# Optimization experiments

Hardware: AMD Instinct MI355X
Metric: run time of the kernel (lower is better)

The kernel has to match this reference:

```python
import jax, jax.numpy as jnp
import numpy as np

B, C, N, T = 32, 32, 512, 168
EMB = 40
K_NEI = 20
ALPHA = 3.0          # saturation rate in graph learning
GCN_DEPTH = 2
PROP_ALPHA = 0.05    # retaining ratio in mix-hop propagation
KERNELS = (2, 3, 6, 7)
DIL = 2
T_OUT = T - (max(KERNELS) - 1) * DIL   # 156
C_BR = C // len(KERNELS)               # 8 channels per inception branch
EPS = 1e-5


def _conv2d(x, w, b, dil):
    # x: (B,Cin,N,T), w: (Cout,Cin,1,k), temporal dilation dil
    y = jax.lax.conv_general_dilated(
        x, w, window_strides=(1, 1), padding='VALID',
        rhs_dilation=(1, dil), dimension_numbers=('NCHW', 'OIHW', 'NCHW'))
    return y + b[None, :, None, None]


def _inception(x, ws, bs):
    outs = [_conv2d(x, w, b, DIL) for w, b in zip(ws, bs)]
    tmin = outs[-1].shape[-1]   # largest kernel -> shortest output
    return jnp.concatenate([o[..., -tmin:] for o in outs], axis=1)


def setup_inputs() -> dict:
    key = jax.random.key(0)
    ks = jax.random.split(key, 32)
    d = {}
    d['x'] = jax.random.normal(ks[0], (B, C, N, T), jnp.float32)
    d['idx'] = jnp.arange(N)  # permutation of nodes (identity)
    # graph learning params
    d['emb1'] = jax.random.normal(ks[1], (N, EMB), jnp.float32)
    d['emb2'] = jax.random.normal(ks[2], (N, EMB), jnp.float32)
    d['W1'] = jax.random.normal(ks[3], (EMB, EMB), jnp.float32) * 0.15
    d['b1'] = jnp.zeros((EMB,), jnp.float32)
    d['W2'] = jax.random.normal(ks[4], (EMB, EMB), jnp.float32) * 0.15
    d['b2'] = jnp.zeros((EMB,), jnp.float32)
    # dilated inception filter/gate conv params
    i = 5
    for pre in ('f', 'g'):
        for k in KERNELS:
            d[f'{pre}w{k}'] = jax.random.normal(ks[i], (C_BR, C, 1, k), jnp.float32) * 0.05
            d[f'{pre}b{k}'] = jnp.zeros((C_BR,), jnp.float32)
            i += 1
    # mix-hop 1x1 mlp: (gcn_depth+1)*C -> C
    d['mlp_w'] = jax.random.normal(ks[i], (C, (GCN_DEPTH + 1) * C, 1, 1), jnp.float32) * 0.05
    d['mlp_b'] = jnp.zeros((C,), jnp.float32)
    # node-indexed layer norm affine params, shape (C, N, T_OUT)
    d['ln_w'] = jnp.ones((C, N, T_OUT), jnp.float32)
    d['ln_b'] = jnp.zeros((C, N, T_OUT), jnp.float32)
    return d


def reference(x, idx, emb1, emb2, W1, b1, W2, b2,
              fw2, fb2, fw3, fb3, fw6, fb6, fw7, fb7,
              gw2, gb2, gw3, gb3, gw6, gb6, gw7, gb7,
              mlp_w, mlp_b, ln_w, ln_b):
    # ---- graph learning: topk-masked adjacency (N,N) ----
    n1 = jnp.tanh(ALPHA * (emb1[idx] @ W1.T + b1))
    n2 = jnp.tanh(ALPHA * (emb2[idx] @ W2.T + b2))
    a = n1 @ n2.T - n2 @ n1.T
    A = jax.nn.relu(jnp.tanh(ALPHA * a))
    _, top_idx = jax.lax.top_k(A, K_NEI)                 # deterministic topk (torch adds rand*0.01 tiebreak)
    mask = jnp.zeros_like(A).at[jnp.arange(A.shape[0])[:, None], top_idx].set(1.0)
    A = A * mask

    # ---- dilated inception gated temporal conv ----
    filt = jnp.tanh(_inception(x, (fw2, fw3, fw6, fw7), (fb2, fb3, fb6, fb7)))
    gate = jax.nn.sigmoid(_inception(x, (gw2, gw3, gw6, gw7), (gb2, gb3, gb6, gb7)))
    z = filt * gate                                       # (B, C, N, T_OUT)

    # ---- mix-hop graph convolution ----
    Ah = A + jnp.eye(A.shape[0], dtype=A.dtype)
    Ah = Ah / Ah.sum(1, keepdims=True)                    # row-degree normalization
    h = z
    hops = [z]
    for _ in range(GCN_DEPTH):
        h = PROP_ALPHA * z + (1.0 - PROP_ALPHA) * jnp.einsum('bcwt,vw->bcvt', h, Ah)
        hops.append(h)
    h0 = jnp.concatenate(hops, axis=1)                    # (B, 3C, N, T_OUT)
    out = _conv2d(h0, mlp_w, mlp_b, 1)                    # 1x1 mlp -> (B, C, N, T_OUT)

    # ---- residual + node-indexed layer norm over dims (C,N,T) ----
    out = out + x[..., -T_OUT:]
    mean = out.mean(axis=(1, 2, 3), keepdims=True)
    var = out.var(axis=(1, 2, 3), keepdims=True)
    out = (out - mean) * jax.lax.rsqrt(var + EPS)
    out = out * ln_w[:, idx, :][None] + ln_b[:, idx, :][None]
    return out
```

## Files before the change

kernel.cpp:

```cpp
#include <hip/hip_runtime.h>

#define NB 32
#define NC 32
#define NNODE 512
#define NT 168
#define NTO 156
#define NQ 39
#define NEMB 40
#define KNEI 20
#define NADJ 21
#define ZT_PITCH 42
#define XROWS 176
#define NPB 4
#define CT (NC * NTO)
#define NPAIR (CT / 8)

static_assert(NTO == 4 * NQ, "t quads");

typedef __attribute__((ext_vector_type(8))) short bf16x8;
typedef __attribute__((ext_vector_type(16))) float f32x16;
typedef __attribute__((ext_vector_type(4))) float f32x4;
typedef __attribute__((ext_vector_type(8))) unsigned short u16x8;

__device__ __forceinline__ float fast_tanh(float x) {
  float e = __expf(2.0f * x);
  return 1.0f - 2.0f / (e + 1.0f);
}
__device__ __forceinline__ float fast_sigmoid(float x) {
  return 1.0f / (1.0f + __expf(-x));
}
__device__ __forceinline__ unsigned short f2b(float v) {
  unsigned int u = __float_as_uint(v);
  unsigned int r = (u + 0x7FFFu + ((u >> 16) & 1u)) >> 16;
  return (unsigned short)r;
}
__device__ __forceinline__ float b2f(unsigned short u) {
  return __uint_as_float((unsigned int)u << 16);
}
template <typename T>
__device__ __forceinline__ void pin(T& v) {
  f32x4 t = __builtin_bit_cast(f32x4, v);
  asm volatile("" : "+v"(t));
  v = __builtin_bit_cast(T, t);
}

__global__ __launch_bounds__(128) void g1_kernel(
    const float* __restrict__ emb1, const float* __restrict__ emb2,
    const float* __restrict__ W1, const float* __restrict__ b1,
    const float* __restrict__ W2, const float* __restrict__ b2,
    const int* __restrict__ idx, float* __restrict__ n1, float* __restrict__ n2) {
  const int v = blockIdx.x;
  const int tid = threadIdx.x;
  const int iv = idx[v];
  if (tid < NEMB) {
    float s = b1[tid];
    const float* er = emb1 + iv * NEMB;
    const float* wr = W1 + tid * NEMB;
    for (int f = 0; f < NEMB; ++f) s = fmaf(er[f], wr[f], s);
    n1[v * NEMB + tid] = tanhf(3.0f * s);
  } else if (tid >= 64 && tid < 64 + NEMB) {
    const int e = tid - 64;
    float s = b2[e];
    const float* er = emb2 + iv * NEMB;
    const float* wr = W2 + e * NEMB;
    for (int f = 0; f < NEMB; ++f) s = fmaf(er[f], wr[f], s);
    n2[v * NEMB + e] = tanhf(3.0f * s);
  }
}

__global__ __launch_bounds__(256) void g2_kernel(
    const float* __restrict__ n1, const float* __restrict__ n2,
    int* __restrict__ cols, float* __restrict__ wts) {
  const int v = blockIdx.x;
  const int tid = threadIdx.x;
  volatile __shared__ float Arow[NNODE];
  __shared__ float n1v[NEMB], n2v[NEMB];
  if (tid < NEMB) n1v[tid] = n1[v * NEMB + tid];
  if (tid >= 64 && tid < 64 + NEMB) n2v[tid - 64] = n2[v * NEMB + tid - 64];
  __syncthreads();
  for (int w = tid; w < NNODE; w += 256) {
    float d1 = 0.f, d2 = 0.f;
    const float* r1 = n1 + w * NEMB;
    const float* r2 = n2 + w * NEMB;
    for (int e = 0; e < NEMB; ++e) {
      d1 = fmaf(n1v[e], r2[e], d1);
      d2 = fmaf(n2v[e], r1[e], d2);
    }
    float a = tanhf(3.0f * (d1 - d2));
    Arow[w] = a > 0.f ? a : 0.f;
  }
  __syncthreads();
  if (tid >= 64) return;
  float sum = 1.0f;
  float selv[KNEI];
  int seli[KNEI];
  #pragma unroll
  for (int s = 0; s < KNEI; ++s) {
    float bv = -1.f; int bi = NNODE;
    #pragma unroll
    for (int w8 = 0; w8 < NNODE / 64; ++w8) {
      const int w = tid + 64 * w8;
      const float val = Arow[w];
      if (val > bv || (val == bv && w < bi)) { bv = val; bi = w; }
    }
    #pragma unroll
    for (int off = 32; off >= 1; off >>= 1) {
      const float ov = __shfl_down(bv, off);
      const int oi = __shfl_down(bi, off);
      if (ov > bv || (ov == bv && oi < bi)) { bv = ov; bi = oi; }
    }
    bv = __shfl(bv, 0);
    bi = __shfl(bi, 0);
    selv[s] = bv;
    seli[s] = bi;
    Arow[bi] = -2.f;
    sum += bv;
  }
  if (tid == 0) {
    const float inv = 1.0f / sum;
    #pragma unroll
    for (int s = 0; s < KNEI; ++s) {
      cols[v * NADJ + s] = seli[s];
      wts[v * NADJ + s] = selv[s] * inv;
    }
    cols[v * NADJ + KNEI] = v;
    wts[v * NADJ + KNEI] = inv;
  }
}

struct ZParams {
  const float* fw[4]; const float* fb[4];
  const float* gw[4]; const float* gb[4];
};

#define PA_CNT (2 * 2 * 7 * 64 * 8)
#define PB_CNT (2 * 64 * 16)
#define PNA_CNT (3 * 2 * 64 * 8)
__global__ __launch_bounds__(256) void pack_kernel(ZParams p, const float* __restrict__ mw,
                                                   unsigned short* __restrict__ pA,
                                                   float* __restrict__ pB,
                                                   unsigned short* __restrict__ pNA) {
  const int idx = blockIdx.x * 256 + threadIdx.x;
  if (idx < PA_CNT) {
    const int e = idx & 7;
    const int l = (idx >> 3) & 63;
    int rest = idx >> 9;
    const int j = rest % 7;
    rest /= 7;
    const int s = rest & 1;
    const int m = rest >> 1;
    const int row = l & 31;
    const int k = ((l >> 5) << 3) + e;
    const int ci = s * 16 + k;
    const int isF = (row < 16);
    const int co = m * 16 + (isF ? row : row - 16);
    const int br = co >> 3;
    const int kk = (br == 0) ? 2 : (br == 1) ? 3 : (br == 2) ? 6 : 7;
    const int jw = j - (7 - kk);
    const float* arr = isF ? p.fw[br] : p.gw[br];
    float val = (jw >= 0) ? arr[((co & 7) * NC + ci) * kk + jw] : 0.f;
    pA[idx] = f2b(val);
  } else if (idx < PA_CNT + PB_CNT) {
    const int ib = idx - PA_CNT;
    const int r = ib & 15;
    const int l = (ib >> 4) & 63;
    const int m = ib >> 10;
    const int rr = r & 7;
    const int row = (rr & 3) + 8 * (rr >> 2) + 4 * (l >> 5);
    const int co = m * 16 + row;
    const int br = co >> 3;
    const float* arr = (r < 8) ? p.fb[br] : p.gb[br];
    pB[ib] = arr[co & 7];
  } else if (idx < PA_CNT + PB_CNT + PNA_CNT) {
    const int in_ = idx - (PA_CNT + PB_CNT);
    const int e = in_ & 7;
    const int l = (in_ >> 3) & 63;
    const int s = (in_ >> 9) & 1;
    const int which = in_ >> 10;
    const int co = l & 31;
    const int c = s * 16 + ((l >> 5) << 3) + e;
    const float w0 = mw[co * 96 + c];
    const float w1 = mw[co * 96 + 32 + c];
    const float w2 = mw[co * 96 + 64 + c];
    float val;
    if (which == 0)      val = w0 + 0.05f * (w1 + w2);
    else if (which == 1) val = 0.95f * w1 + 0.0475f * w2;
    else                 val = 0.9025f * w2;
    pNA[in_] = f2b(val);
  }
}

__global__ __launch_bounds__(256) void xprep_kernel(
    const float* __restrict__ x, unsigned short* __restrict__ xbf) {
  const int n = blockIdx.x;
  const int b = blockIdx.y;
  const int tid = threadIdx.x;
  const int cp = tid & 15;
  const int t0 = tid >> 4;
  const float* xc0 = x + ((size_t)(b * NC + 2 * cp) * NNODE + n) * NT;
  const float* xc1 = xc0 + (size_t)NNODE * NT;
  unsigned int* dst = (unsigned int*)(xbf + (size_t)(b * NNODE + n) * (XROWS * NC));
  #pragma unroll
  for (int k = 0; k < 11; ++k) {
    const int t = t0 + 16 * k;
    unsigned int v = 0;
    if (t < NT) {
      v = (unsigned int)f2b(xc0[t]) | ((unsigned int)f2b(xc1[t]) << 16);
    }
    dst[t * 16 + cp] = v;
  }
}

__attribute__((amdgpu_waves_per_eu(2)))
__global__ __launch_bounds__(256) void conv_kernel(
    const unsigned short* __restrict__ xbf, const unsigned short* __restrict__ pA,
    const float* __restrict__ pBias, unsigned short* __restrict__ z) {
  __shared__ unsigned short zt[NTO * ZT_PITCH];
  const int n0 = blockIdx.x * NPB;
  const int b = blockIdx.y;
  const int tid = threadIdx.x;
  const int w = tid >> 6, l = tid & 63;
  const int jc = l & 31, h = l >> 5;
  const int m = w & 1;

  bf16x8 aF[2][7];
  #pragma unroll
  for (int s = 0; s < 2; ++s)
    #pragma unroll
    for (int j = 0; j < 7; ++j) {
      aF[s][j] = *reinterpret_cast<const bf16x8*>(
          pA + ((((m * 2 + s) * 7 + j) << 6) + l) * 8);
      pin(aF[s][j]);
    }
  f32x4 bias4[4];
  {
    const f32x4* pb4 = reinterpret_cast<const f32x4*>(pBias + (m * 64 + l) * 16);
    #pragma unroll
    for (int q = 0; q < 4; ++q) { bias4[q] = pb4[q]; pin(bias4[q]); }
  }

  for (int nn = 0; nn < NPB; ++nn) {
    const int n = n0 + nn;
    const unsigned short* xbn = xbf + (size_t)(b * NNODE + n) * (XROWS * NC);
    for (int tile = (w >> 1); tile < 5; tile += 2) {
      const int t0 = tile * 32;
      f32x16 acc;
      #pragma unroll
      for (int r = 0; r < 16; ++r) acc[r] = bias4[r >> 2][r & 3];
      const unsigned short* bp = xbn + (t0 + jc) * NC + h * 8;
      #pragma unroll
      for (int j = 0; j < 7; ++j) {
        bf16x8 b0 = *reinterpret_cast<const bf16x8*>(bp + 2 * j * NC);
        bf16x8 b1 = *reinterpret_cast<const bf16x8*>(bp + 2 * j * NC + 16);
        acc = __builtin_amdgcn_mfma_f32_32x32x16_bf16(aF[0][j], b0, acc, 0, 0, 0);
        acc = __builtin_amdgcn_mfma_f32_32x32x16_bf16(aF[1][j], b1, acc, 0, 0, 0);
      }
      const int t = t0 + jc;
      if (t < NTO) {
        #pragma unroll
        for (int r = 0; r < 8; ++r) {
          const float f = fast_tanh(acc[r]);
          const float g = fast_sigmoid(acc[r + 8]);
          const int row = (r & 3) + 8 * (r >> 2) + 4 * h;
          const int co = m * 16 + row;
          zt[t * ZT_PITCH + co] = f2b(f * g);
        }
      }
    }
    __syncthreads();
    unsigned short* zv = z + (size_t)(b * NNODE + n) * CT;
    for (int i = tid; i < CT / 4; i += 256) {
      const int row = i >> 3, q = i & 7;
      ushort4 v4 = *reinterpret_cast<const ushort4*>(zt + row * ZT_PITCH + 4 * q);
      *reinterpret_cast<ushort4*>(zv + 4 * i) = v4;
    }
    __syncthreads();
  }
}

__global__ __launch_bounds__(256) void hop_kernel(
    const unsigned short* __restrict__ src, const int* __restrict__ cols,
    const float* __restrict__ wts, unsigned short* __restrict__ dst) {
  const int bid = blockIdx.x;
  const int v = bid & (NNODE - 1);
  const int b = bid >> 9;
  const int tid = threadIdx.x;
  float acc[3][8];
  #pragma unroll
  for (int k = 0; k < 3; ++k)
    #pragma unroll
    for (int j = 0; j < 8; ++j) acc[k][j] = 0.f;
  for (int s = 0; s < NADJ; ++s) {
    const int col = cols[v * NADJ + s];
    const float w = wts[v * NADJ + s];
    const unsigned short* p = src + ((size_t)(b << 9) + col) * CT;
    #pragma unroll
    for (int k = 0; k < 2; ++k) {
      u16x8 u = *reinterpret_cast<const u16x8*>(p + 8 * (tid + 256 * k));
      #pragma unroll
      for (int j = 0; j < 8; ++j) acc[k][j] = fmaf(w, b2f(u[j]), acc[k][j]);
    }
    if (tid < NPAIR - 512) {
      u16x8 u = *reinterpret_cast<const u16x8*>(p + 8 * (tid + 512));
      #pragma unroll
      for (int j = 0; j < 8; ++j) acc[2][j] = fmaf(w, b2f(u[j]), acc[2][j]);
    }
  }
  unsigned short* dp = dst + ((size_t)(b << 9) + v) * CT;
  #pragma unroll
  for (int k = 0; k < 2; ++k) {
    u16x8 o;
    #pragma unroll
    for (int j = 0; j < 8; ++j) o[j] = f2b(acc[k][j]);
    *reinterpret_cast<u16x8*>(dp + 8 * (tid + 256 * k)) = o;
  }
  if (tid < NPAIR - 512) {
    u16x8 o;
    #pragma unroll
    for (int j = 0; j < 8; ++j) o[j] = f2b(acc[2][j]);
    *reinterpret_cast<u16x8*>(dp + 8 * (tid + 512)) = o;
  }
}

__global__ __launch_bounds__(256) void fin_kernel(
    const unsigned short* __restrict__ z, const unsigned short* __restrict__ g1,
    const unsigned short* __restrict__ g2, const float* __restrict__ x,
    const unsigned short* __restrict__ pNA, const float* __restrict__ mb,
    unsigned short* __restrict__ P, float* __restrict__ stats) {
  const int b = blockIdx.y;
  const int tid = threadIdx.x;
  const int w = tid >> 6, l = tid & 63;
  const int jc = l & 31, h = l >> 5;
  const int v = blockIdx.x * 4 + w;

  bf16x8 nA[3][2];
  #pragma unroll
  for (int which = 0; which < 3; ++which)
    #pragma unroll
    for (int s = 0; s < 2; ++s) {
      nA[which][s] = *reinterpret_cast<const bf16x8*>(
          pNA + (((which * 2 + s) << 6) + l) * 8);
      pin(nA[which][s]);
    }
  float mbr[16];
  #pragma unroll
  for (int r = 0; r < 16; ++r) {
    const int co = (r & 3) + 8 * (r >> 2) + 4 * h;
    mbr[r] = mb[co];
  }

  const size_t base = (size_t)(b << 9) + v;
  const unsigned short* zs_ = z + base * CT;
  const unsigned short* g1s = g1 + base * CT;
  const unsigned short* g2s = g2 + base * CT;
  unsigned short* Ps = P + base * CT;
  float st1 = 0.f, st2 = 0.f;

  #pragma unroll
  for (int tile = 0; tile < 5; ++tile) {
    const int t = tile * 32 + jc;
    const int off = t * NC + h * 8;
    f32x16 acc;
    #pragma unroll
    for (int r = 0; r < 16; ++r) acc[r] = 0.f;
    {
      bf16x8 b0 = *reinterpret_cast<const bf16x8*>(zs_ + off);
      bf16x8 b1 = *reinterpret_cast<const bf16x8*>(zs_ + off + 16);
      acc = __builtin_amdgcn_mfma_f32_32x32x16_bf16(nA[0][0], b0, acc, 0, 0, 0);
      acc = __builtin_amdgcn_mfma_f32_32x32x16_bf16(nA[0][1], b1, acc, 0, 0, 0);
    }
    {
      bf16x8 b0 = *reinterpret_cast<const bf16x8*>(g1s + off);
      bf16x8 b1 = *reinterpret_cast<const bf16x8*>(g1s + off + 16);
      acc = __builtin_amdgcn_mfma_f32_32x32x16_bf16(nA[1][0], b0, acc, 0, 0, 0);
      acc = __builtin_amdgcn_mfma_f32_32x32x16_bf16(nA[1][1], b1, acc, 0, 0, 0);
    }
    {
      bf16x8 b0 = *reinterpret_cast<const bf16x8*>(g2s + off);
      bf16x8 b1 = *reinterpret_cast<const bf16x8*>(g2s + off + 16);
      acc = __builtin_amdgcn_mfma_f32_32x32x16_bf16(nA[2][0], b0, acc, 0, 0, 0);
      acc = __builtin_amdgcn_mfma_f32_32x32x16_bf16(nA[2][1], b1, acc, 0, 0, 0);
    }
    if (t < NTO) {
      #pragma unroll
      for (int r = 0; r < 16; ++r) {
        const int co = (r & 3) + 8 * (r >> 2) + 4 * h;
        const float xr = x[((size_t)(b * NC + co) * NNODE + v) * NT + 12 + t];
        const float val = acc[r] + mbr[r] + xr;
        Ps[co * NTO + t] = f2b(val);
        st1 += val;
        st2 += val * val;
      }
    }
  }
  #pragma unroll
  for (int off = 32; off >= 1; off >>= 1) {
    st1 += __shfl_down(st1, off);
    st2 += __shfl_down(st2, off);
  }
  __shared__ float r1[4], r2[4];
  if ((tid & 63) == 0) { r1[w] = st1; r2[w] = st2; }
  __syncthreads();
  if (tid == 0) {
    atomicAdd(&stats[b * 2], r1[0] + r1[1] + r1[2] + r1[3]);
    atomicAdd(&stats[b * 2 + 1], r2[0] + r2[1] + r2[2] + r2[3]);
  }
}

__global__ __launch_bounds__(256) void ln_kernel(
    const unsigned short* __restrict__ P, float* __restrict__ out,
    const float* __restrict__ lnw, const float* __restrict__ lnb,
    const int* __restrict__ idx, const float* __restrict__ stats) {
  const int i = blockIdx.x * 256 + threadIdx.x;
  const int q = i % NQ;
  const int r = i / NQ;
  const int co = r % NC;
  const int r2 = r / NC;
  const int v = r2 % NNODE;
  const int b = r2 / NNODE;
  const float invM = 1.0f / (float)(NC * NNODE * NTO);
  const float mean = stats[b * 2] * invM;
  const float var = stats[b * 2 + 1] * invM - mean * mean;
  const float rs = rsqrtf(var + 1e-5f);
  ushort4 u = *reinterpret_cast<const ushort4*>(P + 4 * i);
  const int iv = idx[v];
  const int lb = (co * NNODE + iv) * NTO + 4 * q;
  const float4 w = *reinterpret_cast<const float4*>(lnw + lb);
  const float4 bb = *reinterpret_cast<const float4*>(lnb + lb);
  float4 o;
  o.x = (b2f(u.x) - mean) * rs * w.x + bb.x;
  o.y = (b2f(u.y) - mean) * rs * w.y + bb.y;
  o.z = (b2f(u.z) - mean) * rs * w.z + bb.z;
  o.w = (b2f(u.w) - mean) * rs * w.w + bb.w;
  const int ob = ((b * NC + co) * NNODE + v) * NTO + 4 * q;
  *reinterpret_cast<float4*>(out + ob) = o;
}

extern "C" void kernel_launch(void* const* d_in, const int* in_sizes, int n_in,
                              void* d_out, int out_size, void* d_ws, size_t ws_size,
                              hipStream_t stream) {
  const float* x    = (const float*)d_in[0];
  const int*   idx  = (const int*)d_in[1];
  const float* emb1 = (const float*)d_in[2];
  const float* emb2 = (const float*)d_in[3];
  const float* W1   = (const float*)d_in[4];
  const float* b1   = (const float*)d_in[5];
  const float* W2   = (const float*)d_in[6];
  const float* b2   = (const float*)d_in[7];
  const float* mlp_w = (const float*)d_in[24];
  const float* mlp_b = (const float*)d_in[25];
  const float* ln_w = (const float*)d_in[26];
  const float* ln_b = (const float*)d_in[27];

  char* ws = (char*)d_ws;
  float* n1    = (float*)(ws);
  float* n2    = (float*)(ws + (128 << 10));
  int*   cols  = (int*)  (ws + (256 << 10));
  float* wts   = (float*)(ws + (320 << 10));
  float* stats = (float*)(ws + (384 << 10));
  unsigned short* pA = (unsigned short*)(ws + (400 << 10));
  float* pBias = (float*)(ws + (440 << 10));
  unsigned short* pNA = (unsigned short*)(ws + (456 << 10));
  unsigned short* xbf = (unsigned short*)(ws + (512 << 10));
  const size_t xbf_elems = (size_t)NB * NNODE * XROWS * NC;
  const size_t slab_elems = (size_t)NB * NNODE * CT;
  unsigned short* z  = xbf + xbf_elems;
  unsigned short* g1 = z + slab_elems;
  unsigned short* g2 = g1 + slab_elems;
  unsigned short* P  = xbf;

  ZParams zp;
  for (int k = 0; k < 4; ++k) {
    zp.fw[k] = (const float*)d_in[8 + 2 * k];
    zp.fb[k] = (const float*)d_in[9 + 2 * k];
    zp.gw[k] = (const float*)d_in[16 + 2 * k];
    zp.gb[k] = (const float*)d_in[17 + 2 * k];
  }

  hipMemsetAsync(stats, 0, 2 * NB * sizeof(float), stream);
  g1_kernel<<<NNODE, 128, 0, stream>>>(emb1, emb2, W1, b1, W2, b2, idx, n1, n2);
  g2_kernel<<<NNODE, 256, 0, stream>>>(n1, n2, cols, wts);
  pack_kernel<<<76, 256, 0, stream>>>(zp, mlp_w, pA, pBias, pNA);
  xprep_kernel<<<dim3(NNODE, NB), 256, 0, stream>>>(x, xbf);
  conv_kernel<<<dim3(NNODE / NPB, NB), 256, 0, stream>>>(xbf, pA, pBias, z);
  hop_kernel<<<NB * NNODE, 256, 0, stream>>>(z, cols, wts, g1);
  hop_kernel<<<NB * NNODE, 256, 0, stream>>>(g1, cols, wts, g2);
  fin_kernel<<<dim3(NNODE / 4, NB), 256, 0, stream>>>(z, g1, g2, x, pNA, mlp_b,
                                                      P, stats);
  ln_kernel<<<NB * NC * NNODE * NQ / 256, 256, 0, stream>>>(P, (float*)d_out, ln_w,
                                                            ln_b, idx, stats);
}
```

Before: 1.378 ms.

## Reuse layer-norm affine params across batches and reorder hop block mapping

ln_kernel now loads each ln_w/ln_b vector once and loops over all batches, cutting redundant reads of the node-indexed affine parameters. hop_kernel remaps block ids so consecutive blocks handle the same node for eight batches, improving cache locality of the adjacency tables. fin_kernel keeps the MLP bias in shared memory instead of 16 registers and adds an occupancy hint. The per-thread serial batch loop in ln_kernel cuts the grid to 1/32 of its size, which may reduce latency hiding.

```diff
diff --git a/kernel.cpp b/kernel.cpp
--- a/kernel.cpp
+++ b/kernel.cpp
@@ -282,8 +282,11 @@
     const unsigned short* __restrict__ src, const int* __restrict__ cols,
     const float* __restrict__ wts, unsigned short* __restrict__ dst) {
   const int bid = blockIdx.x;
-  const int v = bid & (NNODE - 1);
-  const int b = bid >> 9;
+  const int r = bid & 7;
+  const int t_ = bid >> 3;
+  const int v = t_ & (NNODE - 1);
+  const int g = t_ >> 9;
+  const int b = g * 8 + r;
   const int tid = threadIdx.x;
   float acc[3][8];
   #pragma unroll
@@ -322,7 +325,7 @@
   }
 }
 
-__global__ __launch_bounds__(256) void fin_kernel(
+__global__ __launch_bounds__(256, 8) void fin_kernel(
     const unsigned short* __restrict__ z, const unsigned short* __restrict__ g1,
     const unsigned short* __restrict__ g2, const float* __restrict__ x,
     const unsigned short* __restrict__ pNA, const float* __restrict__ mb,
@@ -332,6 +335,9 @@
   const int w = tid >> 6, l = tid & 63;
   const int jc = l & 31, h = l >> 5;
   const int v = blockIdx.x * 4 + w;
+  __shared__ float mbs[NC];
+  if (tid < NC) mbs[tid] = mb[tid];
+  __syncthreads();
 
   bf16x8 nA[3][2];
   #pragma unroll
@@ -342,12 +348,6 @@
           pNA + (((which * 2 + s) << 6) + l) * 8);
       pin(nA[which][s]);
     }
-  float mbr[16];
-  #pragma unroll
-  for (int r = 0; r < 16; ++r) {
-    const int co = (r & 3) + 8 * (r >> 2) + 4 * h;
-    mbr[r] = mb[co];
-  }
 
   const size_t base = (size_t)(b << 9) + v;
   const unsigned short* zs_ = z + base * CT;
@@ -386,7 +386,7 @@
       for (int r = 0; r < 16; ++r) {
         const int co = (r & 3) + 8 * (r >> 2) + 4 * h;
         const float xr = x[((size_t)(b * NC + co) * NNODE + v) * NT + 12 + t];
-        const float val = acc[r] + mbr[r] + xr;
+        const float val = acc[r] + mbs[co] + xr;
         Ps[co * NTO + t] = f2b(val);
         st1 += val;
         st2 += val * val;
@@ -415,25 +415,26 @@
   const int q = i % NQ;
   const int r = i / NQ;
   const int co = r % NC;
-  const int r2 = r / NC;
-  const int v = r2 % NNODE;
-  const int b = r2 / NNODE;
-  const float invM = 1.0f / (float)(NC * NNODE * NTO);
-  const float mean = stats[b * 2] * invM;
-  const float var = stats[b * 2 + 1] * invM - mean * mean;
-  const float rs = rsqrtf(var + 1e-5f);
-  ushort4 u = *reinterpret_cast<const ushort4*>(P + 4 * i);
+  const int v = r / NC;
   const int iv = idx[v];
   const int lb = (co * NNODE + iv) * NTO + 4 * q;
   const float4 w = *reinterpret_cast<const float4*>(lnw + lb);
   const float4 bb = *reinterpret_cast<const float4*>(lnb + lb);
-  float4 o;
-  o.x = (b2f(u.x) - mean) * rs * w.x + bb.x;
-  o.y = (b2f(u.y) - mean) * rs * w.y + bb.y;
-  o.z = (b2f(u.z) - mean) * rs * w.z + bb.z;
-  o.w = (b2f(u.w) - mean) * rs * w.w + bb.w;
-  const int ob = ((b * NC + co) * NNODE + v) * NTO + 4 * q;
-  *reinterpret_cast<float4*>(out + ob) = o;
+  const float invM = 1.0f / (float)(NC * NNODE * NTO);
+  const int poff = (v * NC + co) * NTO + 4 * q;
+  const int ooff = (co * NNODE + v) * NTO + 4 * q;
+  for (int b = 0; b < NB; ++b) {
+    const float mean = stats[b * 2] * invM;
+    const float var = stats[b * 2 + 1] * invM - mean * mean;
+    const float rs = rsqrtf(var + 1e-5f);
+    ushort4 u = *reinterpret_cast<const ushort4*>(P + (size_t)b * (NNODE * CT) + poff);
+    float4 o;
+    o.x = (b2f(u.x) - mean) * rs * w.x + bb.x;
+    o.y = (b2f(u.y) - mean) * rs * w.y + bb.y;
+    o.z = (b2f(u.z) - mean) * rs * w.z + bb.z;
+    o.w = (b2f(u.w) - mean) * rs * w.w + bb.w;
+    *reinterpret_cast<float4*>(out + (size_t)b * (NC * NNODE * NTO) + ooff) = o;
+  }
 }
 
 extern "C" void kernel_launch(void* const* d_in, const int* in_sizes, int n_in,
@@ -487,6 +488,6 @@
   hop_kernel<<<NB * NNODE, 256, 0, stream>>>(g1, cols, wts, g2);
   fin_kernel<<<dim3(NNODE / 4, NB), 256, 0, stream>>>(z, g1, g2, x, pNA, mlp_b,
                                                       P, stats);
-  ln_kernel<<<NB * NC * NNODE * NQ / 256, 256, 0, stream>>>(P, (float*)d_out, ln_w,
-                                                            ln_b, idx, stats);
-}
+  ln_kernel<<<NNODE * NC * NQ / 256, 256, 0, stream>>>(P, (float*)d_out, ln_w,
+                                                       ln_b, idx, stats);
+}
```

New measurement: 1.822 ms, median of 2. 1.32x slower.
